# Performance work log

Hardware: AMD Instinct MI355X
Metric: run time of the kernel (lower is better)

Reference implementation:

```python
import jax, jax.numpy as jnp
import numpy as np
import math

D_MODEL = 512
N_HEADS = 8
WINDOW = 32
B, L, S = 4, 2048, 2048


def setup_inputs() -> dict:
    key = jax.random.key(0)
    ks = jax.random.split(key, 12)
    scale = 1.0 / math.sqrt(D_MODEL)
    inp = {
        "queries": jax.random.normal(ks[0], (B, L, D_MODEL), jnp.float32),
        "keys": jax.random.normal(ks[1], (B, S, D_MODEL), jnp.float32),
        "values": jax.random.normal(ks[2], (B, S, D_MODEL), jnp.float32),
        # TriangularCausalMask: True above the diagonal => masked
        "attn_mask": jnp.triu(jnp.ones((L, S), jnp.bool_), k=1)[None, None],
        "Wq": jax.random.normal(ks[3], (D_MODEL, D_MODEL), jnp.float32) * scale,
        "bq": jnp.zeros((D_MODEL,), jnp.float32),
        "Wk": jax.random.normal(ks[4], (D_MODEL, D_MODEL), jnp.float32) * scale,
        "bk": jnp.zeros((D_MODEL,), jnp.float32),
        "Wv": jax.random.normal(ks[5], (D_MODEL, D_MODEL), jnp.float32) * scale,
        "bv": jnp.zeros((D_MODEL,), jnp.float32),
        "Wo": jax.random.normal(ks[6], (D_MODEL, D_MODEL), jnp.float32) * scale,
        "bo": jnp.zeros((D_MODEL,), jnp.float32),
        "gamma": jnp.ones((1,), jnp.float32) * 0.5,
    }
    return inp


def reference(queries, keys, values, attn_mask, Wq, bq, Wk, bk, Wv, bv, Wo, bo, gamma):
    Bq, Lq, _ = queries.shape
    Sq = keys.shape[1]
    H = N_HEADS
    q = (queries @ Wq + bq).reshape(Bq, Lq, H, -1)  # [B,L,H,dk]
    k = (keys @ Wk + bk).reshape(Bq, Sq, H, -1)
    v = (values @ Wv + bv).reshape(Bq, Sq, H, -1)

    scores = jnp.einsum('blhd,bshd->bhls', q, k) / math.sqrt(D_MODEL)  # [B,H,L,S]

    # exponential decay on relative position
    rel = jnp.arange(Lq)[:, None] - jnp.arange(Sq)[None, :]  # [L,S]
    decay = jnp.exp(-gamma[0] * jnp.abs(rel).astype(scores.dtype))
    scores = scores * decay[None, None]

    # sliding-window mask (exact replica of _create_window_mask)
    t = jnp.arange(Lq)
    start = jnp.clip(t - WINDOW // 2, 0, None)
    end = jnp.clip(t + WINDOW // 2 + 1, None, Sq)
    wmask = (t[:, None] >= start[None, :]) & (t[:, None] < end[None, :])  # [L,S]
    neg_inf = jnp.asarray(-jnp.inf, scores.dtype)
    scores = jnp.where(wmask[None, None], scores, neg_inf)

    # causal mask: True = masked
    scores = jnp.where(attn_mask, neg_inf, scores)

    attn = jax.nn.softmax(scores, axis=-1)  # dropout is identity at eval
    context = jnp.einsum('bhls,bshd->blhd', attn, v).reshape(Bq, Lq, -1)
    out = context @ Wo + bo
    return (out, attn)
```

## Files before the change

### kernel.cpp

```cpp
#include <hip/hip_runtime.h>
#include <hip/hip_bf16.h>
#include <cstdint>
#include <cstddef>

#define D_MODEL 512
#define N_HEADS 8
#define HDIM 64
#define SEQ 2048
#define B_SZ 4
#define M_TOT (B_SZ * SEQ)
#define ATTN_ROWS (B_SZ * N_HEADS * SEQ)
#define PROJ_ELEMS ((size_t)M_TOT * D_MODEL)

typedef __bf16 bf16x8 __attribute__((ext_vector_type(8)));
typedef float  f32x4  __attribute__((ext_vector_type(4)));

__device__ __forceinline__ unsigned short f2bf(float x) {
    __bf16 b = (__bf16)x;
    return __builtin_bit_cast(unsigned short, b);
}
__device__ __forceinline__ float bf2f(unsigned short u) {
    __bf16 b = __builtin_bit_cast(__bf16, u);
    return (float)b;
}

struct TransArgs {
    const float* W[4];
    unsigned short* Wt[4];
};

__global__ void transpose_k(TransArgs ta) {
    __shared__ float tile[32][33];
    const int z = blockIdx.z;
    const float* W = ta.W[z];
    unsigned short* Wt = ta.Wt[z];
    int x = blockIdx.x * 32 + threadIdx.x;
    int y0 = blockIdx.y * 32;
    for (int j = threadIdx.y; j < 32; j += 8)
        tile[j][threadIdx.x] = W[(size_t)(y0 + j) * D_MODEL + x];
    __syncthreads();
    int xo = blockIdx.y * 32 + threadIdx.x;
    int yo0 = blockIdx.x * 32;
    for (int j = threadIdx.y; j < 32; j += 8)
        Wt[(size_t)(yo0 + j) * D_MODEL + xo] = f2bf(tile[threadIdx.x][j]);
}

struct GemmArgs {
    const float* A[3];
    const unsigned short* Wt[3];
    const float* bias[3];
    void* C[3];
};

#define LDSTRIDE 72

template <int F32OUT>
__global__ __launch_bounds__(256, 2) void gemm_bt(GemmArgs ga) {
    __shared__ __align__(16) unsigned short lsA[128 * LDSTRIDE];
    __shared__ __align__(16) unsigned short lsB[128 * LDSTRIDE];

    const int f = blockIdx.x;
    const int z = f >> 8;
    const int xt = ((f >> 5) & 7) * 8 + (f & 7);
    const int yt = (f >> 3) & 3;
    const float* __restrict__ A           = ga.A[z];
    const unsigned short* __restrict__ Wt = ga.Wt[z];
    const float* __restrict__ bias        = ga.bias[z];

    const int m0 = xt * 128;
    const int n0 = yt * 128;
    const int tid = threadIdx.x;
    const int lane = tid & 63;
    const int wid = tid >> 6;
    const int wm = (wid >> 1) * 64;
    const int wn = (wid & 1) * 64;
    const int lrow = lane & 15;
    const int quad = lane >> 4;

    f32x4 acc[4][4];
#pragma unroll
    for (int i = 0; i < 4; ++i)
#pragma unroll
        for (int j = 0; j < 4; ++j)
            acc[i][j] = (f32x4){0.f, 0.f, 0.f, 0.f};

    for (int kt = 0; kt < D_MODEL; kt += 64) {
        __syncthreads();
#pragma unroll
        for (int p = 0; p < 4; ++p) {
            int c = p * 256 + tid;
            int r = c >> 3;
            int col = (c & 7) << 3;
            const float* src = &A[(size_t)(m0 + r) * D_MODEL + kt + col];
            float4 a0 = *(const float4*)src;
            float4 a1 = *(const float4*)(src + 4);
            unsigned short t8[8];
            t8[0] = f2bf(a0.x); t8[1] = f2bf(a0.y); t8[2] = f2bf(a0.z); t8[3] = f2bf(a0.w);
            t8[4] = f2bf(a1.x); t8[5] = f2bf(a1.y); t8[6] = f2bf(a1.z); t8[7] = f2bf(a1.w);
            *(uint4*)&lsA[r * LDSTRIDE + col] = *(const uint4*)t8;
        }
#pragma unroll
        for (int p = 0; p < 4; ++p) {
            int c = p * 256 + tid;
            int r = c >> 3;
            int col = (c & 7) << 3;
            *(uint4*)&lsB[r * LDSTRIDE + col] =
                *(const uint4*)&Wt[(size_t)(n0 + r) * D_MODEL + kt + col];
        }
        __syncthreads();
#pragma unroll
        for (int ks = 0; ks < 2; ++ks) {
            const int ko = ks * 32 + quad * 8;
            bf16x8 af[4], bfr[4];
#pragma unroll
            for (int mt = 0; mt < 4; ++mt)
                af[mt] = *(const bf16x8*)&lsA[(wm + mt * 16 + lrow) * LDSTRIDE + ko];
#pragma unroll
            for (int nt = 0; nt < 4; ++nt)
                bfr[nt] = *(const bf16x8*)&lsB[(wn + nt * 16 + lrow) * LDSTRIDE + ko];
#pragma unroll
            for (int mt = 0; mt < 4; ++mt)
#pragma unroll
                for (int nt = 0; nt < 4; ++nt)
                    acc[mt][nt] = __builtin_amdgcn_mfma_f32_16x16x32_bf16(
                        af[mt], bfr[nt], acc[mt][nt], 0, 0, 0);
        }
    }

#pragma unroll
    for (int nt = 0; nt < 4; ++nt) {
        const int gcol = n0 + wn + nt * 16 + lrow;
        const float bv = bias[gcol];
#pragma unroll
        for (int mt = 0; mt < 4; ++mt) {
            const int grow = m0 + wm + mt * 16 + quad * 4;
#pragma unroll
            for (int r = 0; r < 4; ++r) {
                const float v = acc[mt][nt][r] + bv;
                if (F32OUT) {
                    __builtin_nontemporal_store(
                        v, &((float*)ga.C[z])[(size_t)(grow + r) * D_MODEL + gcol]);
                } else {
                    ((unsigned short*)ga.C[z])[(size_t)(grow + r) * D_MODEL + gcol] = f2bf(v);
                }
            }
        }
    }
}

#define KV_ROWS 80
#define LROW 72

__device__ __forceinline__ void load16f(const unsigned short* p, float* out) {
    bf16x8 a = *(const bf16x8*)p;
    bf16x8 b = *(const bf16x8*)(p + 8);
#pragma unroll
    for (int i = 0; i < 8; ++i) { out[i] = (float)a[i]; out[8 + i] = (float)b[i]; }
}

__global__ __launch_bounds__(256, 4) void attn2_k(
    const unsigned short* __restrict__ Q,
    const unsigned short* __restrict__ K,
    const unsigned short* __restrict__ V,
    const float* __restrict__ gamma_p,
    float* __restrict__ attn_out,
    float* __restrict__ ctx) {
    __shared__ __align__(16) unsigned short lk[KV_ROWS * LROW];
    __shared__ __align__(16) unsigned short lv[KV_ROWS * LROW];
    __shared__ float pband[64][20];

    const int bh = blockIdx.y;
    const int t0 = blockIdx.x * 64;
    const int b = bh >> 3;
    const int h = bh & 7;
    const int tid = threadIdx.x;
    const int w = tid >> 6;
    const int lane = tid & 63;
    const int r = lane >> 2;
    const int c = lane & 3;

    const float g = gamma_p[0];
    const float rs = 0.044194173824159216f;

    const size_t srcbase = (size_t)b * SEQ * D_MODEL + (size_t)h * HDIM;
    for (int idx = tid; idx < KV_ROWS * 8; idx += 256) {
        const int row = idx >> 3;
        const int ch = (idx & 7) * 8;
        const int grow = t0 - 16 + row;
        uint4 kv4 = {0, 0, 0, 0};
        uint4 vv4 = {0, 0, 0, 0};
        if (grow >= 0) {
            const size_t off = srcbase + (size_t)grow * D_MODEL + ch;
            kv4 = *(const uint4*)&K[off];
            vv4 = *(const uint4*)&V[off];
        }
        *(uint4*)&lk[row * LROW + ch] = kv4;
        *(uint4*)&lv[row * LROW + ch] = vv4;
    }
    __syncthreads();

    const int gr = t0 + w * 16 + r;
    const size_t qoff = srcbase + (size_t)gr * D_MODEL + c * 16;
    float qv[16];
    load16f(&Q[qoff], qv);

    const int lr0 = w * 16 + r;
    float scr[17];
#pragma unroll
    for (int j = 0; j < 17; ++j) {
        float kvv[16];
        load16f(&lk[(lr0 + j) * LROW + c * 16], kvv);
        float part = 0.f;
#pragma unroll
        for (int i = 0; i < 16; ++i) part = fmaf(qv[i], kvv[i], part);
        part += __shfl_xor(part, 1, 64);
        part += __shfl_xor(part, 2, 64);
        const float dec = __expf(-g * (float)(16 - j));
        scr[j] = part * rs * dec;
        if (gr - 16 + j < 0) scr[j] = -__builtin_inff();
    }

    float m = scr[0];
#pragma unroll
    for (int j = 1; j < 17; ++j) m = fmaxf(m, scr[j]);
    float l = 0.f;
#pragma unroll
    for (int j = 0; j < 17; ++j) { scr[j] = __expf(scr[j] - m); l += scr[j]; }
    const float inv = 1.f / l;

    float acc[16];
#pragma unroll
    for (int i = 0; i < 16; ++i) acc[i] = 0.f;
#pragma unroll
    for (int j = 0; j < 17; ++j) {
        float vv[16];
        load16f(&lv[(lr0 + j) * LROW + c * 16], vv);
#pragma unroll
        for (int i = 0; i < 16; ++i) acc[i] = fmaf(scr[j], vv[i], acc[i]);
    }

    float* cp = &ctx[qoff];
#pragma unroll
    for (int i = 0; i < 16; i += 4) {
        f32x4 v = {acc[i] * inv, acc[i + 1] * inv, acc[i + 2] * inv, acc[i + 3] * inv};
        *(f32x4*)&cp[i] = v;
    }

    for (int j = c; j < 17; j += 4) pband[lr0][j] = scr[j] * inv;
    __syncthreads();

    const size_t rowbase = ((size_t)bh * SEQ + t0) * SEQ;
    for (int i = tid; i < 64 * 512; i += 256) {
        const int row = i >> 9;
        const int c4 = i & 511;
        const int t = t0 + row;
        const int s_lo = (t - 16 < 0) ? 0 : t - 16;
        const int lo4 = s_lo >> 2;
        const int hi4 = t >> 2;
        f32x4 v = {0.f, 0.f, 0.f, 0.f};
        if ((unsigned)(c4 - lo4) <= (unsigned)(hi4 - lo4)) {
            const int col0 = c4 * 4;
#pragma unroll
            for (int k = 0; k < 4; ++k) {
                const int col = col0 + k;
                v[k] = (col >= s_lo && col <= t) ? pband[row][col - (t - 16)] : 0.f;
            }
        }
        __builtin_nontemporal_store(
            v, (f32x4*)&attn_out[rowbase + (size_t)row * SEQ + (c4 << 2)]);
    }
}

extern "C" void kernel_launch(void* const* d_in, const int* in_sizes, int n_in,
                              void* d_out, int out_size, void* d_ws, size_t ws_size,
                              hipStream_t stream) {
    const float* queries = (const float*)d_in[0];
    const float* keys    = (const float*)d_in[1];
    const float* values  = (const float*)d_in[2];
    const float* Wq = (const float*)d_in[4];
    const float* bq = (const float*)d_in[5];
    const float* Wk = (const float*)d_in[6];
    const float* bk = (const float*)d_in[7];
    const float* Wv = (const float*)d_in[8];
    const float* bv = (const float*)d_in[9];
    const float* Wo = (const float*)d_in[10];
    const float* bo = (const float*)d_in[11];
    const float* gamma = (const float*)d_in[12];

    char* ws = (char*)d_ws;
    unsigned short* Qp  = (unsigned short*)ws;
    unsigned short* Kp  = Qp + PROJ_ELEMS;
    unsigned short* Vp  = Kp + PROJ_ELEMS;
    unsigned short* WT  = Vp + PROJ_ELEMS;
    unsigned short* WqT = WT;
    unsigned short* WkT = WT + 262144;
    unsigned short* WvT = WT + 2 * 262144;
    unsigned short* WoT = WT + 3 * 262144;
    float* Ctx = (float*)(WT + 4 * 262144);

    float* out_p  = (float*)d_out;
    float* attn_p = out_p + PROJ_ELEMS;

    TransArgs ta;
    ta.W[0] = Wq;  ta.W[1] = Wk;  ta.W[2] = Wv;  ta.W[3] = Wo;
    ta.Wt[0] = WqT; ta.Wt[1] = WkT; ta.Wt[2] = WvT; ta.Wt[3] = WoT;
    transpose_k<<<dim3(16, 16, 4), dim3(32, 8), 0, stream>>>(ta);

    GemmArgs gq;
    gq.A[0] = queries; gq.A[1] = keys;  gq.A[2] = values;
    gq.Wt[0] = WqT;    gq.Wt[1] = WkT;  gq.Wt[2] = WvT;
    gq.bias[0] = bq;   gq.bias[1] = bk; gq.bias[2] = bv;
    gq.C[0] = Qp;      gq.C[1] = Kp;    gq.C[2] = Vp;
    gemm_bt<0><<<768, 256, 0, stream>>>(gq);

    attn2_k<<<dim3(SEQ / 64, B_SZ * N_HEADS), 256, 0, stream>>>(
        Qp, Kp, Vp, gamma, attn_p, Ctx);

    GemmArgs go;
    go.A[0] = Ctx;   go.Wt[0] = WoT; go.bias[0] = bo; go.C[0] = out_p;
    go.A[1] = Ctx;   go.Wt[1] = WoT; go.bias[1] = bo; go.C[1] = out_p;
    go.A[2] = Ctx;   go.Wt[2] = WoT; go.bias[2] = bo; go.C[2] = out_p;
    gemm_bt<1><<<256, 256, 0, stream>>>(go);
}
```

Baseline: 654.6 us.

## Overlap dense attn-matrix write with output GEMM in one fused launch

The attention kernel no longer writes the full 2048x2048 probability matrix. It stores only the 17-wide band of probabilities per row to a workspace buffer. A new combined kernel runs the output projection GEMM in its first 256 blocks and the dense attn-matrix zero-fill and band scatter in the remaining blocks, so the large bandwidth-bound write overlaps compute-bound GEMM work. The GEMM also drops the LDS staging of the weight tile and reads B fragments straight from global memory. This trades LDS traffic for uncoalesced global loads and adds an extra round trip through the band buffer.

```diff
diff --git a/kernel.cpp b/kernel.cpp
--- a/kernel.cpp
+++ b/kernel.cpp
@@ -45,30 +45,13 @@
         Wt[(size_t)(yo0 + j) * D_MODEL + xo] = f2bf(tile[threadIdx.x][j]);
 }
 
-struct GemmArgs {
-    const float* A[3];
-    const unsigned short* Wt[3];
-    const float* bias[3];
-    void* C[3];
-};
-
 #define LDSTRIDE 72
 
 template <int F32OUT>
-__global__ __launch_bounds__(256, 2) void gemm_bt(GemmArgs ga) {
-    __shared__ __align__(16) unsigned short lsA[128 * LDSTRIDE];
-    __shared__ __align__(16) unsigned short lsB[128 * LDSTRIDE];
-
-    const int f = blockIdx.x;
-    const int z = f >> 8;
-    const int xt = ((f >> 5) & 7) * 8 + (f & 7);
-    const int yt = (f >> 3) & 3;
-    const float* __restrict__ A           = ga.A[z];
-    const unsigned short* __restrict__ Wt = ga.Wt[z];
-    const float* __restrict__ bias        = ga.bias[z];
-
-    const int m0 = xt * 128;
-    const int n0 = yt * 128;
+__device__ __forceinline__ void gemm_tile(
+    const float* __restrict__ A, const unsigned short* __restrict__ Wt,
+    const float* __restrict__ bias, void* __restrict__ C,
+    int m0, int n0, unsigned short* lsA) {
     const int tid = threadIdx.x;
     const int lane = tid & 63;
     const int wid = tid >> 6;
@@ -76,6 +59,11 @@
     const int wn = (wid & 1) * 64;
     const int lrow = lane & 15;
     const int quad = lane >> 4;
+
+    const unsigned short* brow[4];
+#pragma unroll
+    for (int nt = 0; nt < 4; ++nt)
+        brow[nt] = &Wt[(size_t)(n0 + wn + nt * 16 + lrow) * D_MODEL + quad * 8];
 
     f32x4 acc[4][4];
 #pragma unroll
@@ -99,14 +87,6 @@
             t8[4] = f2bf(a1.x); t8[5] = f2bf(a1.y); t8[6] = f2bf(a1.z); t8[7] = f2bf(a1.w);
             *(uint4*)&lsA[r * LDSTRIDE + col] = *(const uint4*)t8;
         }
-#pragma unroll
-        for (int p = 0; p < 4; ++p) {
-            int c = p * 256 + tid;
-            int r = c >> 3;
-            int col = (c & 7) << 3;
-            *(uint4*)&lsB[r * LDSTRIDE + col] =
-                *(const uint4*)&Wt[(size_t)(n0 + r) * D_MODEL + kt + col];
-        }
         __syncthreads();
 #pragma unroll
         for (int ks = 0; ks < 2; ++ks) {
@@ -117,7 +97,7 @@
                 af[mt] = *(const bf16x8*)&lsA[(wm + mt * 16 + lrow) * LDSTRIDE + ko];
 #pragma unroll
             for (int nt = 0; nt < 4; ++nt)
-                bfr[nt] = *(const bf16x8*)&lsB[(wn + nt * 16 + lrow) * LDSTRIDE + ko];
+                bfr[nt] = *(const bf16x8*)&brow[nt][kt + ks * 32];
 #pragma unroll
             for (int mt = 0; mt < 4; ++mt)
 #pragma unroll
@@ -137,15 +117,30 @@
 #pragma unroll
             for (int r = 0; r < 4; ++r) {
                 const float v = acc[mt][nt][r] + bv;
-                if (F32OUT) {
+                if (F32OUT)
                     __builtin_nontemporal_store(
-                        v, &((float*)ga.C[z])[(size_t)(grow + r) * D_MODEL + gcol]);
-                } else {
-                    ((unsigned short*)ga.C[z])[(size_t)(grow + r) * D_MODEL + gcol] = f2bf(v);
-                }
+                        v, &((float*)C)[(size_t)(grow + r) * D_MODEL + gcol]);
+                else
+                    ((unsigned short*)C)[(size_t)(grow + r) * D_MODEL + gcol] = f2bf(v);
             }
         }
     }
+}
+
+struct GemmArgs {
+    const float* A[3];
+    const unsigned short* Wt[3];
+    const float* bias[3];
+    void* C[3];
+};
+
+__global__ __launch_bounds__(256, 2) void gemm_qkv(GemmArgs ga) {
+    __shared__ __align__(16) unsigned short lsA[128 * LDSTRIDE];
+    const int f = blockIdx.x;
+    const int z = f >> 8;
+    const int xt = ((f >> 5) & 7) * 8 + (f & 7);
+    const int yt = (f >> 3) & 3;
+    gemm_tile<0>(ga.A[z], ga.Wt[z], ga.bias[z], ga.C[z], xt * 128, yt * 128, lsA);
 }
 
 #define KV_ROWS 80
@@ -158,16 +153,15 @@
     for (int i = 0; i < 8; ++i) { out[i] = (float)a[i]; out[8 + i] = (float)b[i]; }
 }
 
-__global__ __launch_bounds__(256, 4) void attn2_k(
+__global__ __launch_bounds__(256, 4) void attn3_k(
     const unsigned short* __restrict__ Q,
     const unsigned short* __restrict__ K,
     const unsigned short* __restrict__ V,
     const float* __restrict__ gamma_p,
-    float* __restrict__ attn_out,
+    float* __restrict__ pb,
     float* __restrict__ ctx) {
     __shared__ __align__(16) unsigned short lk[KV_ROWS * LROW];
     __shared__ __align__(16) unsigned short lv[KV_ROWS * LROW];
-    __shared__ float pband[64][20];
 
     const int bh = blockIdx.y;
     const int t0 = blockIdx.x * 64;
@@ -246,10 +240,34 @@
         *(f32x4*)&cp[i] = v;
     }
 
-    for (int j = c; j < 17; j += 4) pband[lr0][j] = scr[j] * inv;
-    __syncthreads();
+    float* prow = &pb[((size_t)bh * SEQ + gr) * 20];
+    for (int j = c; j < 17; j += 4) prow[j] = scr[j] * inv;
+}
+
+__global__ __launch_bounds__(256, 2) void fused_k(
+    const float* __restrict__ Ctx,
+    const unsigned short* __restrict__ WoT,
+    const float* __restrict__ bo,
+    float* __restrict__ out_p,
+    const float* __restrict__ pb,
+    float* __restrict__ attn_out) {
+    __shared__ __align__(16) unsigned short lsA[128 * LDSTRIDE];
+
+    if (blockIdx.x < 256) {
+        const int f = blockIdx.x;
+        const int xt = ((f >> 5) & 7) * 8 + (f & 7);
+        const int yt = (f >> 3) & 3;
+        gemm_tile<1>(Ctx, WoT, bo, out_p, xt * 128, yt * 128, lsA);
+        return;
+    }
+
+    const int wb = blockIdx.x - 256;
+    const int bh = wb >> 5;
+    const int t0 = (wb & 31) * 64;
+    const int tid = threadIdx.x;
 
     const size_t rowbase = ((size_t)bh * SEQ + t0) * SEQ;
+    const size_t prowbase = ((size_t)bh * SEQ + t0) * 20;
     for (int i = tid; i < 64 * 512; i += 256) {
         const int row = i >> 9;
         const int c4 = i & 511;
@@ -259,11 +277,12 @@
         const int hi4 = t >> 2;
         f32x4 v = {0.f, 0.f, 0.f, 0.f};
         if ((unsigned)(c4 - lo4) <= (unsigned)(hi4 - lo4)) {
+            const float* prow = &pb[prowbase + (size_t)row * 20];
             const int col0 = c4 * 4;
 #pragma unroll
             for (int k = 0; k < 4; ++k) {
                 const int col = col0 + k;
-                v[k] = (col >= s_lo && col <= t) ? pband[row][col - (t - 16)] : 0.f;
+                v[k] = (col >= s_lo && col <= t) ? prow[col - (t - 16)] : 0.f;
             }
         }
         __builtin_nontemporal_store(
@@ -297,6 +316,7 @@
     unsigned short* WvT = WT + 2 * 262144;
     unsigned short* WoT = WT + 3 * 262144;
     float* Ctx = (float*)(WT + 4 * 262144);
+    float* pb  = Ctx + PROJ_ELEMS;
 
     float* out_p  = (float*)d_out;
     float* attn_p = out_p + PROJ_ELEMS;
@@ -311,14 +331,10 @@
     gq.Wt[0] = WqT;    gq.Wt[1] = WkT;  gq.Wt[2] = WvT;
     gq.bias[0] = bq;   gq.bias[1] = bk; gq.bias[2] = bv;
     gq.C[0] = Qp;      gq.C[1] = Kp;    gq.C[2] = Vp;
-    gemm_bt<0><<<768, 256, 0, stream>>>(gq);
-
-    attn2_k<<<dim3(SEQ / 64, B_SZ * N_HEADS), 256, 0, stream>>>(
-        Qp, Kp, Vp, gamma, attn_p, Ctx);
-
-    GemmArgs go;
-    go.A[0] = Ctx;   go.Wt[0] = WoT; go.bias[0] = bo; go.C[0] = out_p;
-    go.A[1] = Ctx;   go.Wt[1] = WoT; go.bias[1] = bo; go.C[1] = out_p;
-    go.A[2] = Ctx;   go.Wt[2] = WoT; go.bias[2] = bo; go.C[2] = out_p;
-    gemm_bt<1><<<256, 256, 0, stream>>>(go);
-}
+    gemm_qkv<<<768, 256, 0, stream>>>(gq);
+
+    attn3_k<<<dim3(SEQ / 64, B_SZ * N_HEADS), 256, 0, stream>>>(
+        Qp, Kp, Vp, gamma, pb, Ctx);
+
+    fused_k<<<1280, 256, 0, stream>>>(Ctx, WoT, bo, out_p, pb, attn_p);
+}
```

After: 674.8 us. 1.03x slower.
